# Kernel optimization log

Hardware: AMD Instinct MI355X
Metric: run time of the kernel (lower is better)

The kernel has to match this reference:

```python
import jax, jax.numpy as jnp
import numpy as np
from jax import lax

NUM_SCALES = 3
BASE_WEIGHT = 1.0
BOUNDARY_WEIGHT = 2.0


def _avg_pool3d_same(x, k):
    # F.avg_pool3d(kernel=k, stride=1, padding=k//2, count_include_pad=True)
    # -> window sum with zero padding, divided by constant k**3.
    p = k // 2
    s = lax.reduce_window(
        x, jnp.array(0.0, x.dtype), lax.add,
        window_dimensions=(1, 1, k, k, k),
        window_strides=(1, 1, 1, 1, 1),
        padding=((0, 0), (0, 0), (p, p), (p, p), (p, p)),
    )
    return s / jnp.array(k ** 3, x.dtype)


def setup_inputs() -> dict:
    key = jax.random.key(0)
    k1, k2 = jax.random.split(key)
    logits = jax.random.normal(k1, (2, 2, 96, 192, 192), dtype=jnp.float32)
    labels = jax.random.randint(k2, (2, 1, 96, 192, 192), 0, 2, dtype=jnp.int32)
    return {"logits": logits, "labels": labels}


def reference(logits, labels):
    B, C = logits.shape[0], logits.shape[1]
    labels_sq = labels[:, 0].astype(jnp.int32)              # (B,D,H,W)
    onehot = jax.nn.one_hot(labels_sq, C, dtype=jnp.float32, axis=1)  # (B,C,D,H,W)

    # multi-scale boundary weight map: sum_s sum_c |onehot - avgpool_k(onehot)|
    weight_map = jnp.zeros((B, 1) + logits.shape[2:], dtype=jnp.float32)
    for scale_idx in range(NUM_SCALES):
        k = 3 + 2 * scale_idx
        smoothed = _avg_pool3d_same(onehot, k)
        weight_map = weight_map + jnp.abs(onehot - smoothed).sum(axis=1, keepdims=True)
    w_max = weight_map.max()
    weight_map = jnp.where(w_max > 0, weight_map / w_max, weight_map)

    pixel_weights = BASE_WEIGHT + BOUNDARY_WEIGHT * weight_map[:, 0]  # (B,D,H,W)

    log_probs = jax.nn.log_softmax(logits, axis=1)          # (B,C,D,H,W)
    nll = -jnp.take_along_axis(log_probs, labels_sq[:, None].astype(jnp.int32), axis=1)[:, 0]
    return (nll * pixel_weights).mean()
```

## Files before the change

### kernel.cpp

```cpp
#include <hip/hip_runtime.h>

#define BB 2
#define CC 2
#define DD 96
#define HH 192
#define WW 192
static constexpr int NV   = BB * DD * HH * WW;
static constexpr int HW_  = HH * WW;
static constexpr int DHW_ = DD * HW_;
static constexpr int ROWS = BB * DD * HH;
static constexpr int QPR  = WW / 4;
static constexpr int RPB  = 4;
static constexpr int TPB  = QPR * RPB;
static constexpr int NBLKS = ROWS / RPB;

#define PM1 0x00010001u
#define PM3 0x00030003u
#define PM7 0x00070007u
#define PMF 0x000F000Fu
#define PM1F 0x001F001Fu
#define PM3F 0x003F003Fu

__global__ __launch_bounds__(TPB) void k_xsum(const int* __restrict__ lab,
                                              unsigned short* __restrict__ xs) {
    int t = threadIdx.x;
    int r = t / QPR;
    int q = t - r * QPR;
    int row = blockIdx.x * RPB + r;
    int i0  = row * WW + q * 4;

    const int4* l4 = (const int4*)lab;
    int4 cur = l4[i0 >> 2];
    int4 prv = (q > 0)       ? l4[(i0 >> 2) - 1] : int4{0, 0, 0, 0};
    int4 nxt = (q < QPR - 1) ? l4[(i0 >> 2) + 1] : int4{0, 0, 0, 0};

    int v[12] = {prv.x, prv.y, prv.z, prv.w,
                 cur.x, cur.y, cur.z, cur.w,
                 nxt.x, nxt.y, nxt.z, nxt.w};

    int s7[4], s5[4], s3[4];
    s7[0] = v[1] + v[2] + v[3] + v[4] + v[5] + v[6] + v[7];
#pragma unroll
    for (int j = 0; j < 3; ++j) s7[j + 1] = s7[j] - v[j + 1] + v[j + 8];
#pragma unroll
    for (int j = 0; j < 4; ++j) {
        s5[j] = s7[j] - v[j + 1] - v[j + 7];
        s3[j] = s5[j] - v[j + 2] - v[j + 6];
    }
    unsigned short o[4];
#pragma unroll
    for (int j = 0; j < 4; ++j)
        o[j] = (unsigned short)(v[j + 4] | (s3[j] << 1) | (s5[j] << 3) | (s7[j] << 6));
    *(ushort2*)&o[0];
    uint2 st;
    st.x = (unsigned)o[0] | ((unsigned)o[1] << 16);
    st.y = (unsigned)o[2] | ((unsigned)o[3] << 16);
    *(uint2*)(xs + i0) = st;
}

__device__ __forceinline__ unsigned ypack(const unsigned* g) {
    unsigned t3 = ((g[2] >> 1) & PM3) + ((g[3] >> 1) & PM3) + ((g[4] >> 1) & PM3);
    unsigned t5 = ((g[1] >> 3) & PM7) + ((g[2] >> 3) & PM7) + ((g[3] >> 3) & PM7)
                + ((g[4] >> 3) & PM7) + ((g[5] >> 3) & PM7);
    unsigned t7 = ((g[0] >> 6) & PM7) + ((g[1] >> 6) & PM7) + ((g[2] >> 6) & PM7)
                + ((g[3] >> 6) & PM7) + ((g[4] >> 6) & PM7) + ((g[5] >> 6) & PM7)
                + ((g[6] >> 6) & PM7);
    return (g[3] & PM1) | (t3 << 1) | (t5 << 5) | (t7 << 10);
}

__global__ __launch_bounds__(TPB) void k_ysum(const unsigned short* __restrict__ xs,
                                              unsigned short* __restrict__ ys) {
    int t = threadIdx.x;
    int r = t / QPR;
    int q = t - r * QPR;
    int row = blockIdx.x * RPB + r;
    int h   = row % HH;
    int i0  = row * WW + q * 4;

    unsigned gx[7], gy[7];
#pragma unroll
    for (int k = 0; k < 7; ++k) {
        int hh = h + k - 3;
        if (hh >= 0 && hh < HH) {
            uint2 u = *(const uint2*)(xs + i0 + (k - 3) * WW);
            gx[k] = u.x; gy[k] = u.y;
        } else { gx[k] = 0u; gy[k] = 0u; }
    }
    uint2 st;
    st.x = ypack(gx);
    st.y = ypack(gy);
    *(uint2*)(ys + i0) = st;
}

__global__ __launch_bounds__(TPB) void k_loss(const unsigned short* __restrict__ ys,
                                              const float* __restrict__ logits,
                                              float* __restrict__ p_nll,
                                              float* __restrict__ p_nw,
                                              float* __restrict__ p_wm) {
    int t = threadIdx.x;
    int r = t / QPR;
    int q = t - r * QPR;
    int row = blockIdx.x * RPB + r;
    int h   = row % HH;
    int rd  = row / HH;
    int d   = rd % DD;
    int b   = rd / DD;
    int i0  = row * WW + q * 4;

    unsigned ux[7], uy[7];
#pragma unroll
    for (int k = 0; k < 7; ++k) {
        int dd = d + k - 3;
        if (dd >= 0 && dd < DD) {
            uint2 u = *(const uint2*)(ys + i0 + (k - 3) * HW_);
            ux[k] = u.x; uy[k] = u.y;
        } else { ux[k] = 0u; uy[k] = 0u; }
    }
    unsigned S3x = ((ux[2] >> 1) & PMF) + ((ux[3] >> 1) & PMF) + ((ux[4] >> 1) & PMF);
    unsigned S3y = ((uy[2] >> 1) & PMF) + ((uy[3] >> 1) & PMF) + ((uy[4] >> 1) & PMF);
    unsigned S5x = ((ux[1] >> 5) & PM1F) + ((ux[2] >> 5) & PM1F) + ((ux[3] >> 5) & PM1F)
                 + ((ux[4] >> 5) & PM1F) + ((ux[5] >> 5) & PM1F);
    unsigned S5y = ((uy[1] >> 5) & PM1F) + ((uy[2] >> 5) & PM1F) + ((uy[3] >> 5) & PM1F)
                 + ((uy[4] >> 5) & PM1F) + ((uy[5] >> 5) & PM1F);
    unsigned S7x = ((ux[0] >> 10) & PM3F) + ((ux[1] >> 10) & PM3F) + ((ux[2] >> 10) & PM3F)
                 + ((ux[3] >> 10) & PM3F) + ((ux[4] >> 10) & PM3F) + ((ux[5] >> 10) & PM3F)
                 + ((ux[6] >> 10) & PM3F);
    unsigned S7y = ((uy[0] >> 10) & PM3F) + ((uy[1] >> 10) & PM3F) + ((uy[2] >> 10) & PM3F)
                 + ((uy[3] >> 10) & PM3F) + ((uy[4] >> 10) & PM3F) + ((uy[5] >> 10) & PM3F)
                 + ((uy[6] >> 10) & PM3F);

    int ch3 = 1 + min(h, 1) + min(HH - 1 - h, 1);
    int ch5 = 1 + min(h, 2) + min(HH - 1 - h, 2);
    int ch7 = 1 + min(h, 3) + min(HH - 1 - h, 3);
    int cd3 = 1 + min(d, 1) + min(DD - 1 - d, 1);
    int cd5 = 1 + min(d, 2) + min(DD - 1 - d, 2);
    int cd7 = 1 + min(d, 3) + min(DD - 1 - d, 3);
    int chd3 = ch3 * cd3, chd5 = ch5 * cd5, chd7 = ch7 * cd7;

    const float4 L0 = *(const float4*)(logits + i0 + b * DHW_);
    const float4 L1 = *(const float4*)(logits + i0 + b * DHW_ + DHW_);
    float l0a[4] = {L0.x, L0.y, L0.z, L0.w};
    float l1a[4] = {L1.x, L1.y, L1.z, L1.w};

    float acc_n = 0.f, acc_p = 0.f, mx = 0.f;
#pragma unroll
    for (int j = 0; j < 4; ++j) {
        unsigned w3 = (j < 2) ? ux[3] : uy[3];
        unsigned s3w = (j < 2) ? S3x : S3y;
        unsigned s5w = (j < 2) ? S5x : S5y;
        unsigned s7w = (j < 2) ? S7x : S7y;
        const int sh = (j & 1) * 16;
        int S3 = (int)((s3w >> sh) & 0xFFFFu);
        int S5 = (int)((s5w >> sh) & 0xFFFFu);
        int S7 = (int)((s7w >> sh) & 0xFFFFu);
        int lab = (int)((w3 >> sh) & 1u);

        int w = q * 4 + j;
        int cw3 = 1 + min(w, 1) + min(WW - 1 - w, 1);
        int cw5 = 1 + min(w, 2) + min(WW - 1 - w, 2);
        int cw7 = 1 + min(w, 3) + min(WW - 1 - w, 3);

        float fq = (float)(cw3 * chd3 - 2 * S3) * (1.0f / 27.0f)
                 + (float)(cw5 * chd5 - 2 * S5) * (1.0f / 125.0f)
                 + (float)(cw7 * chd7 - 2 * S7) * (1.0f / 343.0f);
        float wm = lab ? (3.0f + fq) : (3.0f - fq);

        float s  = lab ? (l0a[j] - l1a[j]) : (l1a[j] - l0a[j]);
        float nll = fmaxf(s, 0.f) + __logf(1.0f + __expf(-fabsf(s)));

        acc_n += nll;
        acc_p += nll * wm;
        mx = fmaxf(mx, wm);
    }

#pragma unroll
    for (int off = 32; off > 0; off >>= 1) {
        acc_n += __shfl_down(acc_n, off);
        acc_p += __shfl_down(acc_p, off);
        mx     = fmaxf(mx, __shfl_down(mx, off));
    }
    __shared__ float s_n[3], s_p[3], s_m[3];
    int wid  = threadIdx.x >> 6;
    int lane = threadIdx.x & 63;
    if (lane == 0) { s_n[wid] = acc_n; s_p[wid] = acc_p; s_m[wid] = mx; }
    __syncthreads();
    if (threadIdx.x == 0) {
        float a = s_n[0] + s_n[1] + s_n[2];
        float p = s_p[0] + s_p[1] + s_p[2];
        float m2 = fmaxf(s_m[0], fmaxf(s_m[1], s_m[2]));
        p_nll[blockIdx.x] = a;
        p_nw[blockIdx.x]  = p;
        p_wm[blockIdx.x]  = m2;
    }
}

__global__ __launch_bounds__(256) void k_fin(const float* __restrict__ pn,
                                             const float* __restrict__ pw,
                                             const float* __restrict__ pm,
                                             float* __restrict__ out) {
    double s = 0.0, p = 0.0;
    float mx = 0.f;
    for (int t = threadIdx.x; t < NBLKS; t += 256) {
        s += (double)pn[t];
        p += (double)pw[t];
        mx = fmaxf(mx, pm[t]);
    }
#pragma unroll
    for (int off = 32; off > 0; off >>= 1) {
        s  += __shfl_down(s, off);
        p  += __shfl_down(p, off);
        mx  = fmaxf(mx, __shfl_down(mx, off));
    }
    __shared__ double sh_s[4], sh_p[4];
    __shared__ float  sh_m[4];
    int wid  = threadIdx.x >> 6;
    int lane = threadIdx.x & 63;
    if (lane == 0) { sh_s[wid] = s; sh_p[wid] = p; sh_m[wid] = mx; }
    __syncthreads();
    if (threadIdx.x == 0) {
        double S = 0.0, P = 0.0;
        float  M = 0.f;
#pragma unroll
        for (int t = 0; t < 4; ++t) { S += sh_s[t]; P += sh_p[t]; M = fmaxf(M, sh_m[t]); }
        double res = (M > 0.f) ? (S + 2.0 * P / (double)M) : S;
        out[0] = (float)(res / (double)NV);
    }
}

extern "C" void kernel_launch(void* const* d_in, const int* in_sizes, int n_in,
                              void* d_out, int out_size, void* d_ws, size_t ws_size,
                              hipStream_t stream) {
    const float* logits = (const float*)d_in[0];
    const int*   labels = (const int*)d_in[1];
    float*       out    = (float*)d_out;

    char* ws = (char*)d_ws;
    float* p_nll = (float*)ws;
    float* p_nw  = (float*)(ws + 40960);
    float* p_wm  = (float*)(ws + 81920);
    unsigned short* xs = (unsigned short*)(ws + 131072);
    unsigned short* ys = xs + NV;

    k_xsum<<<NBLKS, TPB, 0, stream>>>(labels, xs);
    k_ysum<<<NBLKS, TPB, 0, stream>>>(xs, ys);
    k_loss<<<NBLKS, TPB, 0, stream>>>(ys, logits, p_nll, p_nw, p_wm);
    k_fin<<<1, 256, 0, stream>>>(p_nll, p_nw, p_wm, out);
}
```

Measured before the change: 51.98 us.

## Fuse W and H box sums into one LDS-staged kernel, widen loss kernel

Result: faster. 43.93 us (-15.5%).

```diff
diff --git a/kernel.cpp b/kernel.cpp
--- a/kernel.cpp
+++ b/kernel.cpp
@@ -10,53 +10,20 @@
 static constexpr int DHW_ = DD * HW_;
 static constexpr int ROWS = BB * DD * HH;
 static constexpr int QPR  = WW / 4;
-static constexpr int RPB  = 4;
-static constexpr int TPB  = QPR * RPB;
-static constexpr int NBLKS = ROWS / RPB;
-
-#define PM1 0x00010001u
-#define PM3 0x00030003u
-#define PM7 0x00070007u
-#define PMF 0x000F000Fu
+
+static constexpr int SEGQ = 8;
+static constexpr int NSEG = QPR / SEGQ;
+static constexpr int LSTR = SEGQ + 1;
+static constexpr int WHBLKS = BB * DD * NSEG;
+
+static constexpr int LBLKS = ROWS / 16;
+
+#define PM1  0x00010001u
+#define PM3  0x00030003u
+#define PM7  0x00070007u
+#define PMF  0x000F000Fu
 #define PM1F 0x001F001Fu
 #define PM3F 0x003F003Fu
-
-__global__ __launch_bounds__(TPB) void k_xsum(const int* __restrict__ lab,
-                                              unsigned short* __restrict__ xs) {
-    int t = threadIdx.x;
-    int r = t / QPR;
-    int q = t - r * QPR;
-    int row = blockIdx.x * RPB + r;
-    int i0  = row * WW + q * 4;
-
-    const int4* l4 = (const int4*)lab;
-    int4 cur = l4[i0 >> 2];
-    int4 prv = (q > 0)       ? l4[(i0 >> 2) - 1] : int4{0, 0, 0, 0};
-    int4 nxt = (q < QPR - 1) ? l4[(i0 >> 2) + 1] : int4{0, 0, 0, 0};
-
-    int v[12] = {prv.x, prv.y, prv.z, prv.w,
-                 cur.x, cur.y, cur.z, cur.w,
-                 nxt.x, nxt.y, nxt.z, nxt.w};
-
-    int s7[4], s5[4], s3[4];
-    s7[0] = v[1] + v[2] + v[3] + v[4] + v[5] + v[6] + v[7];
-#pragma unroll
-    for (int j = 0; j < 3; ++j) s7[j + 1] = s7[j] - v[j + 1] + v[j + 8];
-#pragma unroll
-    for (int j = 0; j < 4; ++j) {
-        s5[j] = s7[j] - v[j + 1] - v[j + 7];
-        s3[j] = s5[j] - v[j + 2] - v[j + 6];
-    }
-    unsigned short o[4];
-#pragma unroll
-    for (int j = 0; j < 4; ++j)
-        o[j] = (unsigned short)(v[j + 4] | (s3[j] << 1) | (s5[j] << 3) | (s7[j] << 6));
-    *(ushort2*)&o[0];
-    uint2 st;
-    st.x = (unsigned)o[0] | ((unsigned)o[1] << 16);
-    st.y = (unsigned)o[2] | ((unsigned)o[3] << 16);
-    *(uint2*)(xs + i0) = st;
-}
 
 __device__ __forceinline__ unsigned ypack(const unsigned* g) {
     unsigned t3 = ((g[2] >> 1) & PM3) + ((g[3] >> 1) & PM3) + ((g[4] >> 1) & PM3);
@@ -68,109 +35,156 @@
     return (g[3] & PM1) | (t3 << 1) | (t5 << 5) | (t7 << 10);
 }
 
-__global__ __launch_bounds__(TPB) void k_ysum(const unsigned short* __restrict__ xs,
-                                              unsigned short* __restrict__ ys) {
-    int t = threadIdx.x;
-    int r = t / QPR;
-    int q = t - r * QPR;
-    int row = blockIdx.x * RPB + r;
-    int h   = row % HH;
-    int i0  = row * WW + q * 4;
-
-    unsigned gx[7], gy[7];
-#pragma unroll
-    for (int k = 0; k < 7; ++k) {
-        int hh = h + k - 3;
-        if (hh >= 0 && hh < HH) {
-            uint2 u = *(const uint2*)(xs + i0 + (k - 3) * WW);
-            gx[k] = u.x; gy[k] = u.y;
-        } else { gx[k] = 0u; gy[k] = 0u; }
-    }
-    uint2 st;
-    st.x = ypack(gx);
-    st.y = ypack(gy);
-    *(uint2*)(ys + i0) = st;
-}
-
-__global__ __launch_bounds__(TPB) void k_loss(const unsigned short* __restrict__ ys,
+__global__ __launch_bounds__(256) void k_wh(const int* __restrict__ lab,
+                                            unsigned short* __restrict__ ys) {
+    __shared__ uint2 lds[HH * LSTR];
+    int blk  = blockIdx.x;
+    int seg  = blk % NSEG;
+    int bd   = blk / NSEG;
+    int base = bd * HW_;
+    const int4* l4 = (const int4*)lab;
+    int bq = base >> 2;
+
+    for (int t = threadIdx.x; t < HH * SEGQ; t += 256) {
+        int row  = t >> 3;
+        int qloc = t & 7;
+        int gq   = seg * SEGQ + qloc;
+        int qi   = bq + row * QPR + gq;
+        int4 cur = l4[qi];
+        int4 prv = (gq > 0)       ? l4[qi - 1] : int4{0, 0, 0, 0};
+        int4 nxt = (gq < QPR - 1) ? l4[qi + 1] : int4{0, 0, 0, 0};
+        int v[12] = {prv.x, prv.y, prv.z, prv.w,
+                     cur.x, cur.y, cur.z, cur.w,
+                     nxt.x, nxt.y, nxt.z, nxt.w};
+        int s7[4], s5[4], s3[4];
+        s7[0] = v[1] + v[2] + v[3] + v[4] + v[5] + v[6] + v[7];
+#pragma unroll
+        for (int j = 0; j < 3; ++j) s7[j + 1] = s7[j] - v[j + 1] + v[j + 8];
+#pragma unroll
+        for (int j = 0; j < 4; ++j) {
+            s5[j] = s7[j] - v[j + 1] - v[j + 7];
+            s3[j] = s5[j] - v[j + 2] - v[j + 6];
+        }
+        unsigned o0 = (unsigned)(v[4] | (s3[0] << 1) | (s5[0] << 3) | (s7[0] << 6));
+        unsigned o1 = (unsigned)(v[5] | (s3[1] << 1) | (s5[1] << 3) | (s7[1] << 6));
+        unsigned o2 = (unsigned)(v[6] | (s3[2] << 1) | (s5[2] << 3) | (s7[2] << 6));
+        unsigned o3 = (unsigned)(v[7] | (s3[3] << 1) | (s5[3] << 3) | (s7[3] << 6));
+        uint2 st;
+        st.x = o0 | (o1 << 16);
+        st.y = o2 | (o3 << 16);
+        lds[row * LSTR + qloc] = st;
+    }
+    __syncthreads();
+
+    for (int t = threadIdx.x; t < HH * SEGQ; t += 256) {
+        int row  = t >> 3;
+        int qloc = t & 7;
+        int gq   = seg * SEGQ + qloc;
+        unsigned gx[7], gy[7];
+#pragma unroll
+        for (int k = 0; k < 7; ++k) {
+            int hh = row + k - 3;
+            if (hh >= 0 && hh < HH) {
+                uint2 u = lds[hh * LSTR + qloc];
+                gx[k] = u.x; gy[k] = u.y;
+            } else { gx[k] = 0u; gy[k] = 0u; }
+        }
+        uint2 st;
+        st.x = ypack(gx);
+        st.y = ypack(gy);
+        *(uint2*)(ys + base + row * WW + gq * 4) = st;
+    }
+}
+
+__global__ __launch_bounds__(192) void k_loss(const unsigned short* __restrict__ ys,
                                               const float* __restrict__ logits,
                                               float* __restrict__ p_nll,
                                               float* __restrict__ p_nw,
                                               float* __restrict__ p_wm) {
-    int t = threadIdx.x;
-    int r = t / QPR;
-    int q = t - r * QPR;
-    int row = blockIdx.x * RPB + r;
-    int h   = row % HH;
-    int rd  = row / HH;
-    int d   = rd % DD;
-    int b   = rd / DD;
-    int i0  = row * WW + q * 4;
-
-    unsigned ux[7], uy[7];
-#pragma unroll
-    for (int k = 0; k < 7; ++k) {
-        int dd = d + k - 3;
-        if (dd >= 0 && dd < DD) {
-            uint2 u = *(const uint2*)(ys + i0 + (k - 3) * HW_);
-            ux[k] = u.x; uy[k] = u.y;
-        } else { ux[k] = 0u; uy[k] = 0u; }
-    }
-    unsigned S3x = ((ux[2] >> 1) & PMF) + ((ux[3] >> 1) & PMF) + ((ux[4] >> 1) & PMF);
-    unsigned S3y = ((uy[2] >> 1) & PMF) + ((uy[3] >> 1) & PMF) + ((uy[4] >> 1) & PMF);
-    unsigned S5x = ((ux[1] >> 5) & PM1F) + ((ux[2] >> 5) & PM1F) + ((ux[3] >> 5) & PM1F)
-                 + ((ux[4] >> 5) & PM1F) + ((ux[5] >> 5) & PM1F);
-    unsigned S5y = ((uy[1] >> 5) & PM1F) + ((uy[2] >> 5) & PM1F) + ((uy[3] >> 5) & PM1F)
-                 + ((uy[4] >> 5) & PM1F) + ((uy[5] >> 5) & PM1F);
-    unsigned S7x = ((ux[0] >> 10) & PM3F) + ((ux[1] >> 10) & PM3F) + ((ux[2] >> 10) & PM3F)
-                 + ((ux[3] >> 10) & PM3F) + ((ux[4] >> 10) & PM3F) + ((ux[5] >> 10) & PM3F)
-                 + ((ux[6] >> 10) & PM3F);
-    unsigned S7y = ((uy[0] >> 10) & PM3F) + ((uy[1] >> 10) & PM3F) + ((uy[2] >> 10) & PM3F)
-                 + ((uy[3] >> 10) & PM3F) + ((uy[4] >> 10) & PM3F) + ((uy[5] >> 10) & PM3F)
-                 + ((uy[6] >> 10) & PM3F);
-
-    int ch3 = 1 + min(h, 1) + min(HH - 1 - h, 1);
-    int ch5 = 1 + min(h, 2) + min(HH - 1 - h, 2);
-    int ch7 = 1 + min(h, 3) + min(HH - 1 - h, 3);
-    int cd3 = 1 + min(d, 1) + min(DD - 1 - d, 1);
-    int cd5 = 1 + min(d, 2) + min(DD - 1 - d, 2);
-    int cd7 = 1 + min(d, 3) + min(DD - 1 - d, 3);
-    int chd3 = ch3 * cd3, chd5 = ch5 * cd5, chd7 = ch7 * cd7;
-
-    const float4 L0 = *(const float4*)(logits + i0 + b * DHW_);
-    const float4 L1 = *(const float4*)(logits + i0 + b * DHW_ + DHW_);
-    float l0a[4] = {L0.x, L0.y, L0.z, L0.w};
-    float l1a[4] = {L1.x, L1.y, L1.z, L1.w};
+    int tid  = threadIdx.x;
+    int rloc = tid / 24;
+    int q8   = tid % 24;
+    bool interior = (q8 > 0) && (q8 < 23);
 
     float acc_n = 0.f, acc_p = 0.f, mx = 0.f;
-#pragma unroll
-    for (int j = 0; j < 4; ++j) {
-        unsigned w3 = (j < 2) ? ux[3] : uy[3];
-        unsigned s3w = (j < 2) ? S3x : S3y;
-        unsigned s5w = (j < 2) ? S5x : S5y;
-        unsigned s7w = (j < 2) ? S7x : S7y;
-        const int sh = (j & 1) * 16;
-        int S3 = (int)((s3w >> sh) & 0xFFFFu);
-        int S5 = (int)((s5w >> sh) & 0xFFFFu);
-        int S7 = (int)((s7w >> sh) & 0xFFFFu);
-        int lab = (int)((w3 >> sh) & 1u);
-
-        int w = q * 4 + j;
-        int cw3 = 1 + min(w, 1) + min(WW - 1 - w, 1);
-        int cw5 = 1 + min(w, 2) + min(WW - 1 - w, 2);
-        int cw7 = 1 + min(w, 3) + min(WW - 1 - w, 3);
-
-        float fq = (float)(cw3 * chd3 - 2 * S3) * (1.0f / 27.0f)
-                 + (float)(cw5 * chd5 - 2 * S5) * (1.0f / 125.0f)
-                 + (float)(cw7 * chd7 - 2 * S7) * (1.0f / 343.0f);
-        float wm = lab ? (3.0f + fq) : (3.0f - fq);
-
-        float s  = lab ? (l0a[j] - l1a[j]) : (l1a[j] - l0a[j]);
-        float nll = fmaxf(s, 0.f) + __logf(1.0f + __expf(-fabsf(s)));
-
-        acc_n += nll;
-        acc_p += nll * wm;
-        mx = fmaxf(mx, wm);
+
+#pragma unroll
+    for (int it = 0; it < 2; ++it) {
+        int row = blockIdx.x * 16 + it * 8 + rloc;
+        int h   = row % HH;
+        int rd  = row / HH;
+        int d   = rd % DD;
+        int b   = rd / DD;
+        int i0  = row * WW + q8 * 8;
+
+        unsigned u[7][4];
+#pragma unroll
+        for (int k = 0; k < 7; ++k) {
+            int dd = d + k - 3;
+            if (dd >= 0 && dd < DD) {
+                uint4 t4 = *(const uint4*)(ys + i0 + (k - 3) * HW_);
+                u[k][0] = t4.x; u[k][1] = t4.y; u[k][2] = t4.z; u[k][3] = t4.w;
+            } else {
+                u[k][0] = 0u; u[k][1] = 0u; u[k][2] = 0u; u[k][3] = 0u;
+            }
+        }
+        unsigned S3[4], S5[4], S7[4];
+#pragma unroll
+        for (int w = 0; w < 4; ++w) {
+            S3[w] = ((u[2][w] >> 1) & PMF) + ((u[3][w] >> 1) & PMF) + ((u[4][w] >> 1) & PMF);
+            S5[w] = ((u[1][w] >> 5) & PM1F) + ((u[2][w] >> 5) & PM1F) + ((u[3][w] >> 5) & PM1F)
+                  + ((u[4][w] >> 5) & PM1F) + ((u[5][w] >> 5) & PM1F);
+            S7[w] = ((u[0][w] >> 10) & PM3F) + ((u[1][w] >> 10) & PM3F) + ((u[2][w] >> 10) & PM3F)
+                  + ((u[3][w] >> 10) & PM3F) + ((u[4][w] >> 10) & PM3F) + ((u[5][w] >> 10) & PM3F)
+                  + ((u[6][w] >> 10) & PM3F);
+        }
+
+        int ch3 = 1 + min(h, 1) + min(HH - 1 - h, 1);
+        int ch5 = 1 + min(h, 2) + min(HH - 1 - h, 2);
+        int ch7 = 1 + min(h, 3) + min(HH - 1 - h, 3);
+        int cd3 = 1 + min(d, 1) + min(DD - 1 - d, 1);
+        int cd5 = 1 + min(d, 2) + min(DD - 1 - d, 2);
+        int cd7 = 1 + min(d, 3) + min(DD - 1 - d, 3);
+        int chd3 = ch3 * cd3, chd5 = ch5 * cd5, chd7 = ch7 * cd7;
+        int i3 = 3 * chd3, i5 = 5 * chd5, i7 = 7 * chd7;
+
+        const float* lp = logits + i0 + b * DHW_;
+        const float4 A0 = *(const float4*)(lp);
+        const float4 A1 = *(const float4*)(lp + 4);
+        const float4 B0 = *(const float4*)(lp + DHW_);
+        const float4 B1 = *(const float4*)(lp + DHW_ + 4);
+        float l0[8] = {A0.x, A0.y, A0.z, A0.w, A1.x, A1.y, A1.z, A1.w};
+        float l1[8] = {B0.x, B0.y, B0.z, B0.w, B1.x, B1.y, B1.z, B1.w};
+
+#pragma unroll
+        for (int j = 0; j < 8; ++j) {
+            const int wd = j >> 1;
+            const int sh = (j & 1) * 16;
+            int S3j  = (int)((S3[wd] >> sh) & 0xFFFFu);
+            int S5j  = (int)((S5[wd] >> sh) & 0xFFFFu);
+            int S7j  = (int)((S7[wd] >> sh) & 0xFFFFu);
+            int labj = (int)((u[3][wd] >> sh) & 1u);
+
+            int c3 = i3, c5 = i5, c7 = i7;
+            if (!interior) {
+                int w = q8 * 8 + j;
+                int cw3 = 1 + min(w, 1) + min(WW - 1 - w, 1);
+                int cw5 = 1 + min(w, 2) + min(WW - 1 - w, 2);
+                int cw7 = 1 + min(w, 3) + min(WW - 1 - w, 3);
+                c3 = cw3 * chd3; c5 = cw5 * chd5; c7 = cw7 * chd7;
+            }
+            float fq = (float)(c3 - 2 * S3j) * (1.0f / 27.0f)
+                     + (float)(c5 - 2 * S5j) * (1.0f / 125.0f)
+                     + (float)(c7 - 2 * S7j) * (1.0f / 343.0f);
+            float sgn = labj ? 1.0f : -1.0f;
+            float wm  = fmaf(sgn, fq, 3.0f);
+            float s   = sgn * (l0[j] - l1[j]);
+            float nll = fmaxf(s, 0.f) + __logf(1.0f + __expf(-fabsf(s)));
+
+            acc_n += nll;
+            acc_p += nll * wm;
+            mx = fmaxf(mx, wm);
+        }
     }
 
 #pragma unroll
@@ -180,17 +194,14 @@
         mx     = fmaxf(mx, __shfl_down(mx, off));
     }
     __shared__ float s_n[3], s_p[3], s_m[3];
-    int wid  = threadIdx.x >> 6;
-    int lane = threadIdx.x & 63;
+    int wid  = tid >> 6;
+    int lane = tid & 63;
     if (lane == 0) { s_n[wid] = acc_n; s_p[wid] = acc_p; s_m[wid] = mx; }
     __syncthreads();
-    if (threadIdx.x == 0) {
-        float a = s_n[0] + s_n[1] + s_n[2];
-        float p = s_p[0] + s_p[1] + s_p[2];
-        float m2 = fmaxf(s_m[0], fmaxf(s_m[1], s_m[2]));
-        p_nll[blockIdx.x] = a;
-        p_nw[blockIdx.x]  = p;
-        p_wm[blockIdx.x]  = m2;
+    if (tid == 0) {
+        p_nll[blockIdx.x] = s_n[0] + s_n[1] + s_n[2];
+        p_nw[blockIdx.x]  = s_p[0] + s_p[1] + s_p[2];
+        p_wm[blockIdx.x]  = fmaxf(s_m[0], fmaxf(s_m[1], s_m[2]));
     }
 }
 
@@ -200,7 +211,7 @@
                                              float* __restrict__ out) {
     double s = 0.0, p = 0.0;
     float mx = 0.f;
-    for (int t = threadIdx.x; t < NBLKS; t += 256) {
+    for (int t = threadIdx.x; t < LBLKS; t += 256) {
         s += (double)pn[t];
         p += (double)pw[t];
         mx = fmaxf(mx, pm[t]);
@@ -236,13 +247,11 @@
 
     char* ws = (char*)d_ws;
     float* p_nll = (float*)ws;
-    float* p_nw  = (float*)(ws + 40960);
-    float* p_wm  = (float*)(ws + 81920);
-    unsigned short* xs = (unsigned short*)(ws + 131072);
-    unsigned short* ys = xs + NV;
-
-    k_xsum<<<NBLKS, TPB, 0, stream>>>(labels, xs);
-    k_ysum<<<NBLKS, TPB, 0, stream>>>(xs, ys);
-    k_loss<<<NBLKS, TPB, 0, stream>>>(ys, logits, p_nll, p_nw, p_wm);
-    k_fin<<<1, 256, 0, stream>>>(p_nll, p_nw, p_wm, out);
-}
+    float* p_nw  = (float*)(ws + 16384);
+    float* p_wm  = (float*)(ws + 32768);
+    unsigned short* ys = (unsigned short*)(ws + 65536);
+
+    k_wh  <<<WHBLKS, 256, 0, stream>>>(labels, ys);
+    k_loss<<<LBLKS, 192, 0, stream>>>(ys, logits, p_nll, p_nw, p_wm);
+    k_fin <<<1, 256, 0, stream>>>(p_nll, p_nw, p_wm, out);
+}
```
